# Performance work log

Hardware: AMD Instinct MI355X
Metric: run time of the kernel (lower is better)

The kernel has to match this reference:

```python
import jax, jax.numpy as jnp
import numpy as np

RESOLUTION = 7
RATIOS = (0.25, 0.125, 0.0625, 0.03125)  # spatial scales for P2..P5
SAMPLE_RATIO = 2
BASE_SIZE = 224.0
BASE_LEVEL = 4.0
LEVEL_MIN = 2.0  # -log2(1/4)
LEVEL_MAX = 5.0  # -log2(1/32)
EPS = 1e-6
IMG = 800.0


def _make_boxes(key, n):
    k1, k2, k3, k4 = jax.random.split(key, 4)
    # log-uniform box sizes in [16, 512] px so rois hit all FPN levels
    w = jnp.exp2(jax.random.uniform(k1, (n,), minval=4.0, maxval=9.0))
    h = jnp.exp2(jax.random.uniform(k2, (n,), minval=4.0, maxval=9.0))
    cx = jax.random.uniform(k3, (n,), minval=0.0, maxval=IMG)
    cy = jax.random.uniform(k4, (n,), minval=0.0, maxval=IMG)
    x1 = jnp.clip(cx - w / 2, 0.0, IMG - 1)
    y1 = jnp.clip(cy - h / 2, 0.0, IMG - 1)
    x2 = jnp.clip(cx + w / 2, 0.0, IMG - 1)
    y2 = jnp.clip(cy + h / 2, 0.0, IMG - 1)
    return jnp.stack([x1, y1, jnp.maximum(x2, x1), jnp.maximum(y2, y1)], axis=1)


def setup_inputs() -> dict:
    key = jax.random.key(0)
    ks = jax.random.split(key, 8)
    N, C = 2, 256
    sizes = [(200, 200), (100, 100), (50, 50), (25, 25), (13, 13)]
    feats = {f"feat{i}": jax.random.normal(ks[i], (N, C, h, w), dtype=jnp.float32)
             for i, (h, w) in enumerate(sizes)}
    feats["props0"] = _make_boxes(ks[5], 512)
    feats["props1"] = _make_boxes(ks[6], 512)
    return feats


def _axis_interp(v, size):
    """Per-axis bilinear setup, matching torchvision RoIAlign (aligned=False)."""
    valid = (v >= -1.0) & (v <= size)
    v0 = jnp.maximum(v, 0.0)
    lo = jnp.floor(v0).astype(jnp.int32)
    at_edge = lo >= size - 1
    lo = jnp.where(at_edge, size - 1, lo)
    hi = jnp.where(at_edge, size - 1, lo + 1)
    frac = jnp.where(at_edge, 0.0, v0 - lo.astype(v.dtype))
    return lo, hi, frac, valid


def _roi_align(feat, rois, scale, res=RESOLUTION, sr=SAMPLE_RATIO):
    """feat: [N,C,H,W], rois: [R,5] (batch_idx,x1,y1,x2,y2) -> [R,C,res,res]."""
    N, C, H, W = feat.shape
    b = rois[:, 0].astype(jnp.int32)
    x1, y1, x2, y2 = (rois[:, 1] * scale, rois[:, 2] * scale,
                      rois[:, 3] * scale, rois[:, 4] * scale)
    roi_w = jnp.maximum(x2 - x1, 1.0)
    roi_h = jnp.maximum(y2 - y1, 1.0)
    bin_w = roi_w / res
    bin_h = roi_h / res
    P = res * sr
    offs = (jnp.arange(P, dtype=jnp.float32) + 0.5) / sr  # sample offsets in bin units
    ys = y1[:, None] + offs[None, :] * bin_h[:, None]  # [R,P]
    xs = x1[:, None] + offs[None, :] * bin_w[:, None]  # [R,P]
    yl, yh, fy, vy = _axis_interp(ys, H)
    xl, xh, fx, vx = _axis_interp(xs, W)
    bi = b[:, None, None]

    def g(yi, xi):  # gather corner values -> [R,P,P,C]
        return feat[bi, :, yi[:, :, None], xi[:, None, :]]

    hy, hx = 1.0 - fy, 1.0 - fx
    val = (g(yl, xl) * (hy[:, :, None] * hx[:, None, :])[..., None]
           + g(yl, xh) * (hy[:, :, None] * fx[:, None, :])[..., None]
           + g(yh, xl) * (fy[:, :, None] * hx[:, None, :])[..., None]
           + g(yh, xh) * (fy[:, :, None] * fx[:, None, :])[..., None])
    val = jnp.where((vy[:, :, None] & vx[:, None, :])[..., None], val, 0.0)
    R = rois.shape[0]
    pooled = val.reshape(R, res, sr, res, sr, C).mean(axis=(2, 4))  # [R,res,res,C]
    return pooled.transpose(0, 3, 1, 2)


def _pool(features, proposals):
    # convert: concat proposals with batch indices -> rois [R,5]
    inds = jnp.concatenate([jnp.full((p.shape[0], 1), i, dtype=p.dtype)
                            for i, p in enumerate(proposals)], axis=0)
    boxes = jnp.concatenate(proposals, axis=0)
    rois = jnp.concatenate([inds, boxes], axis=1)
    rois = jax.lax.stop_gradient(rois)  # torchvision RoIAlign has no roi grad
    # set_level: FPN level assignment (eq.1 of FPN paper)
    areas = (rois[:, 3] - rois[:, 1] + 1) * (rois[:, 4] - rois[:, 2] + 1)
    sizes = jnp.sqrt(areas)
    levels = jnp.floor(BASE_LEVEL + jnp.log2(sizes / BASE_SIZE + EPS))
    levels = (jnp.clip(levels, LEVEL_MIN, LEVEL_MAX) - LEVEL_MIN).astype(jnp.int32)
    R, C = rois.shape[0], features[0].shape[1]
    results = jnp.zeros((R, C, RESOLUTION, RESOLUTION), dtype=boxes.dtype)
    for lvl in range(len(RATIOS)):  # forward uses features[:-1]
        pooled = _roi_align(features[lvl], rois, RATIOS[lvl])
        results = results + jnp.where((levels == lvl)[:, None, None, None], pooled, 0.0)
    return results


def reference(feat0, feat1, feat2, feat3, feat4, props0, props1):
    return _pool([feat0, feat1, feat2, feat3, feat4], [props0, props1])
```

## Files before the change

kernel.cpp:

```cpp
#include <hip/hip_runtime.h>
#include <math.h>

#define C_CH 256
#define RESO 7
#define NBIN 49

__device__ __forceinline__ unsigned short f2bf(float f) {
  unsigned int u = __float_as_uint(f);
  u = (u + 0x7fffu + ((u >> 16) & 1u)) >> 16;
  return (unsigned short)u;
}
__device__ __forceinline__ float bf_lo(unsigned int u) { return __uint_as_float(u << 16); }
__device__ __forceinline__ float bf_hi(unsigned int u) { return __uint_as_float(u & 0xffff0000u); }

struct TArgs {
  const float* src[4];
  unsigned short* dst[4];
  int hw[4];
  int bx0[5];
};

__global__ __launch_bounds__(256) void conv_nhwc_bf16(TArgs a) {
  __shared__ float tile[32][33];
  const int bx = blockIdx.x;
  int l = 0;
  if (bx >= a.bx0[1]) l = 1;
  if (bx >= a.bx0[2]) l = 2;
  if (bx >= a.bx0[3]) l = 3;
  const int HW = a.hw[l];
  const int hw0 = (bx - a.bx0[l]) * 32;
  const int c0 = blockIdx.y * 32;
  const int n = blockIdx.z;

  const float* s = a.src[l] + (size_t)n * C_CH * HW;
  unsigned short* d = a.dst[l] + (size_t)n * HW * C_CH;

  const int tx = threadIdx.x;
  const int ty = threadIdx.y;

  if ((HW & 3) == 0) {
    const int hw = hw0 + tx * 4;
    if (hw + 3 < HW) {
      const float4 v = *(const float4*)(s + (size_t)(c0 + ty) * HW + hw);
      tile[ty][tx * 4 + 0] = v.x;
      tile[ty][tx * 4 + 1] = v.y;
      tile[ty][tx * 4 + 2] = v.z;
      tile[ty][tx * 4 + 3] = v.w;
    } else {
      for (int k = 0; k < 4; ++k)
        if (hw + k < HW) tile[ty][tx * 4 + k] = s[(size_t)(c0 + ty) * HW + hw + k];
    }
  } else {
    for (int k = 0; k < 4; ++k) {
      const int hw = hw0 + tx + 8 * k;
      if (hw < HW) tile[ty][tx + 8 * k] = s[(size_t)(c0 + ty) * HW + hw];
    }
  }
  __syncthreads();

  const int hww = hw0 + ty;
  if (hww < HW) {
    unsigned int lo = (unsigned int)f2bf(tile[tx * 4 + 0][ty]) |
                      ((unsigned int)f2bf(tile[tx * 4 + 1][ty]) << 16);
    unsigned int hi = (unsigned int)f2bf(tile[tx * 4 + 2][ty]) |
                      ((unsigned int)f2bf(tile[tx * 4 + 3][ty]) << 16);
    uint2 v = make_uint2(lo, hi);
    *(uint2*)(d + (size_t)hww * C_CH + c0 + tx * 4) = v;
  }
}

__global__ __launch_bounds__(256) void roi_gather_bf16(
    const unsigned short* __restrict__ f0, const unsigned short* __restrict__ f1,
    const unsigned short* __restrict__ f2, const unsigned short* __restrict__ f3,
    const float* __restrict__ props0, const float* __restrict__ props1,
    float* __restrict__ out) {
  __shared__ float obuf[NBIN * C_CH];
  __shared__ int s_o0[2][14], s_o1[2][14];
  __shared__ float s_w0[2][14], s_w1[2][14];

  const int r = blockIdx.x;
  const int t = threadIdx.x;
  const int b = (r >= 512) ? 1 : 0;
  const float* pr = (b ? props1 : props0) + (r & 511) * 4;
  const float x1 = pr[0], y1 = pr[1], x2 = pr[2], y2 = pr[3];

  const float size = sqrtf((x2 - x1 + 1.0f) * (y2 - y1 + 1.0f));
  float lv = floorf(4.0f + log2f(size / 224.0f + 1e-6f));
  lv = fminf(fmaxf(lv, 2.0f), 5.0f) - 2.0f;
  const int lvl = (int)lv;

  const int Htab[4] = {200, 100, 50, 25};
  const float stab[4] = {0.25f, 0.125f, 0.0625f, 0.03125f};
  const int H = Htab[lvl];
  const int W = H;
  const float sc = stab[lvl];
  const unsigned short* fl = (lvl == 0) ? f0 : (lvl == 1) ? f1 : (lvl == 2) ? f2 : f3;

  const float rx1 = x1 * sc, ry1 = y1 * sc;
  const float roi_w = fmaxf(x2 * sc - rx1, 1.0f);
  const float roi_h = fmaxf(y2 * sc - ry1, 1.0f);
  const float bw = roi_w / 7.0f, bh = roi_h / 7.0f;

  if (t < 28) {
    const int axis = t / 14;
    const int k = t % 14;
    const float off = ((float)k + 0.5f) * 0.5f;
    const float v = axis ? (rx1 + off * bw) : (ry1 + off * bh);
    const int isz = H;
    const bool valid = (v >= -1.0f) && (v <= (float)isz);
    const float v0 = fmaxf(v, 0.0f);
    int lo = (int)floorf(v0);
    const bool edge = (lo >= isz - 1);
    lo = edge ? isz - 1 : lo;
    const int hi = edge ? isz - 1 : lo + 1;
    const float fr = edge ? 0.0f : (v0 - (float)lo);
    const int mul = axis ? C_CH : W * C_CH;
    s_o0[axis][k] = lo * mul;
    s_o1[axis][k] = hi * mul;
    s_w1[axis][k] = valid ? fr : 0.0f;
    s_w0[axis][k] = valid ? (1.0f - fr) : 0.0f;
  }
  __syncthreads();

  const int wv = t >> 6;
  const int ln = t & 63;
  const size_t HWp = (size_t)H * W;

  const unsigned short* base = fl + (size_t)b * HWp * C_CH + ln * 4;
  for (int bb = wv; bb < NBIN; bb += 4) {
    const int ph = bb / 7, pw = bb - ph * 7;
    float4 acc = make_float4(0.f, 0.f, 0.f, 0.f);
#pragma unroll
    for (int s1 = 0; s1 < 2; ++s1) {
      const int sy = 2 * ph + s1;
      const int yo0 = s_o0[0][sy], yo1 = s_o1[0][sy];
      const float wy0 = s_w0[0][sy], wy1 = s_w1[0][sy];
#pragma unroll
      for (int s2 = 0; s2 < 2; ++s2) {
        const int sx = 2 * pw + s2;
        const int xo0 = s_o0[1][sx], xo1 = s_o1[1][sx];
        const float w00 = wy0 * s_w0[1][sx], w01 = wy0 * s_w1[1][sx];
        const float w10 = wy1 * s_w0[1][sx], w11 = wy1 * s_w1[1][sx];
        const uint2 q00 = *(const uint2*)(base + yo0 + xo0);
        const uint2 q01 = *(const uint2*)(base + yo0 + xo1);
        const uint2 q10 = *(const uint2*)(base + yo1 + xo0);
        const uint2 q11 = *(const uint2*)(base + yo1 + xo1);
        acc.x += w00 * bf_lo(q00.x) + w01 * bf_lo(q01.x) + w10 * bf_lo(q10.x) + w11 * bf_lo(q11.x);
        acc.y += w00 * bf_hi(q00.x) + w01 * bf_hi(q01.x) + w10 * bf_hi(q10.x) + w11 * bf_hi(q11.x);
        acc.z += w00 * bf_lo(q00.y) + w01 * bf_lo(q01.y) + w10 * bf_lo(q10.y) + w11 * bf_lo(q11.y);
        acc.w += w00 * bf_hi(q00.y) + w01 * bf_hi(q01.y) + w10 * bf_hi(q10.y) + w11 * bf_hi(q11.y);
      }
    }
    const int c4 = ln * 4;
    obuf[(c4 + 0) * NBIN + bb] = acc.x * 0.25f;
    obuf[(c4 + 1) * NBIN + bb] = acc.y * 0.25f;
    obuf[(c4 + 2) * NBIN + bb] = acc.z * 0.25f;
    obuf[(c4 + 3) * NBIN + bb] = acc.w * 0.25f;
  }
  __syncthreads();

  float4* o4 = (float4*)(out + (size_t)r * (NBIN * C_CH));
  const float4* ob4 = (const float4*)obuf;
  for (int i = t; i < NBIN * C_CH / 4; i += 256) o4[i] = ob4[i];
}

__global__ __launch_bounds__(256) void roi_gather_nchw(
    const float* __restrict__ f0, const float* __restrict__ f1,
    const float* __restrict__ f2, const float* __restrict__ f3,
    const float* __restrict__ props0, const float* __restrict__ props1,
    float* __restrict__ out) {
  __shared__ float obuf[NBIN * C_CH];
  __shared__ int s_o0[2][14], s_o1[2][14];
  __shared__ float s_w0[2][14], s_w1[2][14];

  const int r = blockIdx.x;
  const int t = threadIdx.x;
  const int b = (r >= 512) ? 1 : 0;
  const float* pr = (b ? props1 : props0) + (r & 511) * 4;
  const float x1 = pr[0], y1 = pr[1], x2 = pr[2], y2 = pr[3];
  const float size = sqrtf((x2 - x1 + 1.0f) * (y2 - y1 + 1.0f));
  float lv = floorf(4.0f + log2f(size / 224.0f + 1e-6f));
  lv = fminf(fmaxf(lv, 2.0f), 5.0f) - 2.0f;
  const int lvl = (int)lv;
  const int Htab[4] = {200, 100, 50, 25};
  const float stab[4] = {0.25f, 0.125f, 0.0625f, 0.03125f};
  const int H = Htab[lvl];
  const int W = H;
  const float sc = stab[lvl];
  const float* fl = (lvl == 0) ? f0 : (lvl == 1) ? f1 : (lvl == 2) ? f2 : f3;
  const float rx1 = x1 * sc, ry1 = y1 * sc;
  const float roi_w = fmaxf(x2 * sc - rx1, 1.0f);
  const float roi_h = fmaxf(y2 * sc - ry1, 1.0f);
  const float bw = roi_w / 7.0f, bh = roi_h / 7.0f;
  if (t < 28) {
    const int axis = t / 14;
    const int k = t % 14;
    const float off = ((float)k + 0.5f) * 0.5f;
    const float v = axis ? (rx1 + off * bw) : (ry1 + off * bh);
    const int isz = H;
    const bool valid = (v >= -1.0f) && (v <= (float)isz);
    const float v0 = fmaxf(v, 0.0f);
    int lo = (int)floorf(v0);
    const bool edge = (lo >= isz - 1);
    lo = edge ? isz - 1 : lo;
    const int hi = edge ? isz - 1 : lo + 1;
    const float fr = edge ? 0.0f : (v0 - (float)lo);
    const int mul = axis ? 1 : W;
    s_o0[axis][k] = lo * mul;
    s_o1[axis][k] = hi * mul;
    s_w1[axis][k] = valid ? fr : 0.0f;
    s_w0[axis][k] = valid ? (1.0f - fr) : 0.0f;
  }
  __syncthreads();
  const int wv = t >> 6;
  const int ln = t & 63;
  const size_t HWp = (size_t)H * W;
  const float* base = fl + ((size_t)b * C_CH + ln * 4) * HWp;
  for (int bb = wv; bb < NBIN; bb += 4) {
    const int ph = bb / 7, pw = bb - ph * 7;
    float4 acc = make_float4(0.f, 0.f, 0.f, 0.f);
    for (int s1 = 0; s1 < 2; ++s1) {
      const int sy = 2 * ph + s1;
      const int yo0 = s_o0[0][sy], yo1 = s_o1[0][sy];
      const float wy0 = s_w0[0][sy], wy1 = s_w1[0][sy];
      for (int s2 = 0; s2 < 2; ++s2) {
        const int sx = 2 * pw + s2;
        const int xo0 = s_o0[1][sx], xo1 = s_o1[1][sx];
        const float w00 = wy0 * s_w0[1][sx], w01 = wy0 * s_w1[1][sx];
        const float w10 = wy1 * s_w0[1][sx], w11 = wy1 * s_w1[1][sx];
        float e[4];
        for (int j = 0; j < 4; ++j) {
          e[j] = w00 * base[j * HWp + yo0 + xo0] + w01 * base[j * HWp + yo0 + xo1] +
                 w10 * base[j * HWp + yo1 + xo0] + w11 * base[j * HWp + yo1 + xo1];
        }
        acc.x += e[0]; acc.y += e[1]; acc.z += e[2]; acc.w += e[3];
      }
    }
    const int c4 = ln * 4;
    obuf[(c4 + 0) * NBIN + bb] = acc.x * 0.25f;
    obuf[(c4 + 1) * NBIN + bb] = acc.y * 0.25f;
    obuf[(c4 + 2) * NBIN + bb] = acc.z * 0.25f;
    obuf[(c4 + 3) * NBIN + bb] = acc.w * 0.25f;
  }
  __syncthreads();
  float4* o4 = (float4*)(out + (size_t)r * (NBIN * C_CH));
  const float4* ob4 = (const float4*)obuf;
  for (int i = t; i < NBIN * C_CH / 4; i += 256) o4[i] = ob4[i];
}

extern "C" void kernel_launch(void* const* d_in, const int* in_sizes, int n_in,
                              void* d_out, int out_size, void* d_ws, size_t ws_size,
                              hipStream_t stream) {
  const float* f0 = (const float*)d_in[0];
  const float* f1 = (const float*)d_in[1];
  const float* f2 = (const float*)d_in[2];
  const float* f3 = (const float*)d_in[3];
  const float* p0 = (const float*)d_in[5];
  const float* p1 = (const float*)d_in[6];
  float* out = (float*)d_out;
  unsigned short* ws = (unsigned short*)d_ws;

  const int HWs[4] = {200 * 200, 100 * 100, 50 * 50, 25 * 25};
  size_t off[4];
  size_t acc = 0;
  for (int l = 0; l < 4; ++l) {
    off[l] = acc;
    acc += (size_t)2 * C_CH * HWs[l];
  }
  const size_t need_bytes = acc * sizeof(unsigned short);

  if (ws_size >= need_bytes) {
    TArgs a;
    a.src[0] = f0; a.src[1] = f1; a.src[2] = f2; a.src[3] = f3;
    int cum = 0;
    for (int l = 0; l < 4; ++l) {
      a.dst[l] = ws + off[l];
      a.hw[l] = HWs[l];
      a.bx0[l] = cum;
      cum += (HWs[l] + 31) / 32;
    }
    a.bx0[4] = cum;
    dim3 grid(cum, 8, 2);
    dim3 block(8, 32);
    conv_nhwc_bf16<<<grid, block, 0, stream>>>(a);
    roi_gather_bf16<<<1024, 256, 0, stream>>>(a.dst[0], a.dst[1], a.dst[2], a.dst[3],
                                              p0, p1, out);
  } else {
    roi_gather_nchw<<<1024, 256, 0, stream>>>(f0, f1, f2, f3, p0, p1, out);
  }
}
```

Baseline: 209.4 us.

## Enlarge transpose tiles to 64x64 and widen ROI gather to 512 threads

The NCHW-to-NHWC bf16 conversion kernel now moves 64x64 tiles per block with 256 flat threads, each issuing four float4 loads, so fewer blocks cover the same data. The ROI gather kernel runs with 512 threads (8 waves). Each lane loads 8 bf16 channels via uint4, and the x0/x1 bilinear corners are split across lane halves and combined with a cross-lane shuffle. The goal is wider memory transactions and more parallelism per ROI, at the cost of higher register and LDS use and an extra shuffle per bin.

```diff
diff --git a/kernel.cpp b/kernel.cpp
--- a/kernel.cpp
+++ b/kernel.cpp
@@ -21,55 +21,67 @@
 };
 
 __global__ __launch_bounds__(256) void conv_nhwc_bf16(TArgs a) {
-  __shared__ float tile[32][33];
+  __shared__ float tile[64][65];
   const int bx = blockIdx.x;
   int l = 0;
   if (bx >= a.bx0[1]) l = 1;
   if (bx >= a.bx0[2]) l = 2;
   if (bx >= a.bx0[3]) l = 3;
   const int HW = a.hw[l];
-  const int hw0 = (bx - a.bx0[l]) * 32;
-  const int c0 = blockIdx.y * 32;
+  const int hw0 = (bx - a.bx0[l]) * 64;
+  const int c0 = blockIdx.y * 64;
   const int n = blockIdx.z;
 
   const float* s = a.src[l] + (size_t)n * C_CH * HW;
   unsigned short* d = a.dst[l] + (size_t)n * HW * C_CH;
 
-  const int tx = threadIdx.x;
-  const int ty = threadIdx.y;
-
-  if ((HW & 3) == 0) {
-    const int hw = hw0 + tx * 4;
-    if (hw + 3 < HW) {
-      const float4 v = *(const float4*)(s + (size_t)(c0 + ty) * HW + hw);
-      tile[ty][tx * 4 + 0] = v.x;
-      tile[ty][tx * 4 + 1] = v.y;
-      tile[ty][tx * 4 + 2] = v.z;
-      tile[ty][tx * 4 + 3] = v.w;
-    } else {
-      for (int k = 0; k < 4; ++k)
-        if (hw + k < HW) tile[ty][tx * 4 + k] = s[(size_t)(c0 + ty) * HW + hw + k];
+  const int t = threadIdx.x;
+  const int lane16 = t & 15;
+  const int row16 = t >> 4;
+
+  if (hw0 + 64 <= HW && (HW & 3) == 0) {
+    float4 v[4];
+#pragma unroll
+    for (int i = 0; i < 4; ++i) {
+      const int c_l = row16 + 16 * i;
+      v[i] = *(const float4*)(s + (size_t)(c0 + c_l) * HW + hw0 + lane16 * 4);
+    }
+#pragma unroll
+    for (int i = 0; i < 4; ++i) {
+      const int c_l = row16 + 16 * i;
+      tile[c_l][lane16 * 4 + 0] = v[i].x;
+      tile[c_l][lane16 * 4 + 1] = v[i].y;
+      tile[c_l][lane16 * 4 + 2] = v[i].z;
+      tile[c_l][lane16 * 4 + 3] = v[i].w;
     }
   } else {
-    for (int k = 0; k < 4; ++k) {
-      const int hw = hw0 + tx + 8 * k;
-      if (hw < HW) tile[ty][tx + 8 * k] = s[(size_t)(c0 + ty) * HW + hw];
-    }
-  }
-  __syncthreads();
-
-  const int hww = hw0 + ty;
-  if (hww < HW) {
-    unsigned int lo = (unsigned int)f2bf(tile[tx * 4 + 0][ty]) |
-                      ((unsigned int)f2bf(tile[tx * 4 + 1][ty]) << 16);
-    unsigned int hi = (unsigned int)f2bf(tile[tx * 4 + 2][ty]) |
-                      ((unsigned int)f2bf(tile[tx * 4 + 3][ty]) << 16);
-    uint2 v = make_uint2(lo, hi);
-    *(uint2*)(d + (size_t)hww * C_CH + c0 + tx * 4) = v;
-  }
-}
-
-__global__ __launch_bounds__(256) void roi_gather_bf16(
+    for (int i = 0; i < 4; ++i) {
+      const int c_l = row16 + 16 * i;
+      const float* row = s + (size_t)(c0 + c_l) * HW;
+      for (int k = 0; k < 4; ++k) {
+        const int hw = hw0 + lane16 * 4 + k;
+        tile[c_l][lane16 * 4 + k] = (hw < HW) ? row[hw] : 0.0f;
+      }
+    }
+  }
+  __syncthreads();
+
+#pragma unroll
+  for (int i = 0; i < 4; ++i) {
+    const int hw_l = row16 + 16 * i;
+    const int hww = hw0 + hw_l;
+    if (hww < HW) {
+      const int c4 = lane16 * 4;
+      const unsigned int lo = (unsigned int)f2bf(tile[c4 + 0][hw_l]) |
+                              ((unsigned int)f2bf(tile[c4 + 1][hw_l]) << 16);
+      const unsigned int hi = (unsigned int)f2bf(tile[c4 + 2][hw_l]) |
+                              ((unsigned int)f2bf(tile[c4 + 3][hw_l]) << 16);
+      *(uint2*)(d + (size_t)hww * C_CH + c0 + c4) = make_uint2(lo, hi);
+    }
+  }
+}
+
+__global__ __launch_bounds__(512) void roi_gather_bf16(
     const unsigned short* __restrict__ f0, const unsigned short* __restrict__ f1,
     const unsigned short* __restrict__ f2, const unsigned short* __restrict__ f3,
     const float* __restrict__ props0, const float* __restrict__ props1,
@@ -124,12 +136,14 @@
 
   const int wv = t >> 6;
   const int ln = t & 63;
+  const int cg = ln & 31;
+  const int xt = ln >> 5;
   const size_t HWp = (size_t)H * W;
-
-  const unsigned short* base = fl + (size_t)b * HWp * C_CH + ln * 4;
-  for (int bb = wv; bb < NBIN; bb += 4) {
+  const unsigned short* base = fl + (size_t)b * HWp * C_CH + cg * 8;
+
+  for (int bb = wv; bb < NBIN; bb += 8) {
     const int ph = bb / 7, pw = bb - ph * 7;
-    float4 acc = make_float4(0.f, 0.f, 0.f, 0.f);
+    float acc[8] = {0.f, 0.f, 0.f, 0.f, 0.f, 0.f, 0.f, 0.f};
 #pragma unroll
     for (int s1 = 0; s1 < 2; ++s1) {
       const int sy = 2 * ph + s1;
@@ -138,30 +152,33 @@
 #pragma unroll
       for (int s2 = 0; s2 < 2; ++s2) {
         const int sx = 2 * pw + s2;
-        const int xo0 = s_o0[1][sx], xo1 = s_o1[1][sx];
-        const float w00 = wy0 * s_w0[1][sx], w01 = wy0 * s_w1[1][sx];
-        const float w10 = wy1 * s_w0[1][sx], w11 = wy1 * s_w1[1][sx];
-        const uint2 q00 = *(const uint2*)(base + yo0 + xo0);
-        const uint2 q01 = *(const uint2*)(base + yo0 + xo1);
-        const uint2 q10 = *(const uint2*)(base + yo1 + xo0);
-        const uint2 q11 = *(const uint2*)(base + yo1 + xo1);
-        acc.x += w00 * bf_lo(q00.x) + w01 * bf_lo(q01.x) + w10 * bf_lo(q10.x) + w11 * bf_lo(q11.x);
-        acc.y += w00 * bf_hi(q00.x) + w01 * bf_hi(q01.x) + w10 * bf_hi(q10.x) + w11 * bf_hi(q11.x);
-        acc.z += w00 * bf_lo(q00.y) + w01 * bf_lo(q01.y) + w10 * bf_lo(q10.y) + w11 * bf_lo(q11.y);
-        acc.w += w00 * bf_hi(q00.y) + w01 * bf_hi(q01.y) + w10 * bf_hi(q10.y) + w11 * bf_hi(q11.y);
+        const int xo = xt ? s_o1[1][sx] : s_o0[1][sx];
+        const float wx = xt ? s_w1[1][sx] : s_w0[1][sx];
+        const uint4 q0 = *(const uint4*)(base + yo0 + xo);
+        const uint4 q1 = *(const uint4*)(base + yo1 + xo);
+        const float w0 = wx * wy0, w1 = wx * wy1;
+        acc[0] += w0 * bf_lo(q0.x) + w1 * bf_lo(q1.x);
+        acc[1] += w0 * bf_hi(q0.x) + w1 * bf_hi(q1.x);
+        acc[2] += w0 * bf_lo(q0.y) + w1 * bf_lo(q1.y);
+        acc[3] += w0 * bf_hi(q0.y) + w1 * bf_hi(q1.y);
+        acc[4] += w0 * bf_lo(q0.z) + w1 * bf_lo(q1.z);
+        acc[5] += w0 * bf_hi(q0.z) + w1 * bf_hi(q1.z);
+        acc[6] += w0 * bf_lo(q0.w) + w1 * bf_lo(q1.w);
+        acc[7] += w0 * bf_hi(q0.w) + w1 * bf_hi(q1.w);
       }
     }
-    const int c4 = ln * 4;
-    obuf[(c4 + 0) * NBIN + bb] = acc.x * 0.25f;
-    obuf[(c4 + 1) * NBIN + bb] = acc.y * 0.25f;
-    obuf[(c4 + 2) * NBIN + bb] = acc.z * 0.25f;
-    obuf[(c4 + 3) * NBIN + bb] = acc.w * 0.25f;
+#pragma unroll
+    for (int k = 0; k < 8; ++k) acc[k] += __shfl_xor(acc[k], 32);
+    const int cbase = cg * 8 + xt * 4;
+#pragma unroll
+    for (int k = 0; k < 4; ++k)
+      obuf[(cbase + k) * NBIN + bb] = acc[xt * 4 + k] * 0.25f;
   }
   __syncthreads();
 
   float4* o4 = (float4*)(out + (size_t)r * (NBIN * C_CH));
   const float4* ob4 = (const float4*)obuf;
-  for (int i = t; i < NBIN * C_CH / 4; i += 256) o4[i] = ob4[i];
+  for (int i = t; i < NBIN * C_CH / 4; i += 512) o4[i] = ob4[i];
 }
 
 __global__ __launch_bounds__(256) void roi_gather_nchw(
@@ -277,13 +294,13 @@
       a.dst[l] = ws + off[l];
       a.hw[l] = HWs[l];
       a.bx0[l] = cum;
-      cum += (HWs[l] + 31) / 32;
+      cum += (HWs[l] + 63) / 64;
     }
     a.bx0[4] = cum;
-    dim3 grid(cum, 8, 2);
-    dim3 block(8, 32);
+    dim3 grid(cum, 4, 2);
+    dim3 block(256);
     conv_nhwc_bf16<<<grid, block, 0, stream>>>(a);
-    roi_gather_bf16<<<1024, 256, 0, stream>>>(a.dst[0], a.dst[1], a.dst[2], a.dst[3],
+    roi_gather_bf16<<<1024, 512, 0, stream>>>(a.dst[0], a.dst[1], a.dst[2], a.dst[3],
                                               p0, p1, out);
   } else {
     roi_gather_nchw<<<1024, 256, 0, stream>>>(f0, f1, f2, f3, p0, p1, out);
```

After: 200.5 us. -4.2%, faster.
